# Optimization experiments

Measured on AMD Instinct MI355X. Metric: run time of the kernel, lower is better.

The kernel has to match this reference:

```python
import jax, jax.numpy as jnp
import numpy as np

B, L, C, D = 4, 128, 1024, 512

def setup_inputs() -> dict:
    key = jax.random.key(0)
    ks = jax.random.split(key, 6)
    scale = 1.0 / np.sqrt(D)
    return {
        "hidden": jax.random.normal(ks[0], (B, L, D), dtype=jnp.float32),
        "ctx": jax.random.normal(ks[1], (B, C, D), dtype=jnp.float32),
        "W": jax.random.normal(ks[2], (D, D), dtype=jnp.float32) * scale,
        "U": jax.random.normal(ks[3], (D, D), dtype=jnp.float32) * scale,
        "U_b": jax.random.normal(ks[4], (D,), dtype=jnp.float32) * scale,
        "V": jax.random.normal(ks[5], (D,), dtype=jnp.float32) * scale,
    }

def reference(hidden, ctx, W, U, U_b, V):
    # Bahdanau additive attention: softmax_j V . tanh(W h_i + U c_j + b)
    wq = jnp.einsum('bld,ed->ble', hidden, W)          # [B, L, D]
    uc = jnp.einsum('bcd,ed->bce', ctx, U) + U_b       # [B, C, D]
    s = jnp.tanh(wq[:, :, None, :] + uc[:, None, :, :])  # [B, L, C, D]
    align = jnp.einsum('blcd,d->blc', s, V)            # [B, L, C]
    return jax.nn.softmax(align, axis=-1)
```

## Files before the change

kernel.cpp:

```cpp
#include <hip/hip_runtime.h>
#include <hip/hip_bf16.h>


#define SCALE2 2.8853900817779268f
#define PART (4 * 128 * 1024)

typedef _Float16 f16x8 __attribute__((ext_vector_type(8)));
typedef float f32x4 __attribute__((ext_vector_type(4)));

__device__ __forceinline__ void gload16(const void* g, void* l) {
    __builtin_amdgcn_global_load_lds(
        (const __attribute__((address_space(1))) void*)g,
        (__attribute__((address_space(3))) void*)l,
        16, 0, 0);
}

__global__ __launch_bounds__(256) void gemm_mfma(
    const float* __restrict__ hidden, const float* __restrict__ ctx,
    const float* __restrict__ Wmat, const float* __restrict__ Umat,
    const float* __restrict__ U_b,
    float* __restrict__ ewq_t, float* __restrict__ euc_t)
{
    __shared__ __align__(16) _Float16 Xh[2][64][40];
    __shared__ __align__(16) _Float16 Xl[2][64][40];
    __shared__ __align__(16) _Float16 Wh[2][64][40];
    __shared__ __align__(16) _Float16 Wl[2][64][40];

    const int tid  = threadIdx.x;
    const int lane = tid & 63;
    const int w    = tid >> 6;

    const float *X, *Wm, *bias;
    float* Ct;
    int m0, crow0, Mb, bshift;
    {
        int gb = blockIdx.x;
        if (gb < 64) {
            m0 = (gb & 7) * 64; crow0 = (gb >> 3) * 64;
            X = hidden; Wm = Wmat; bias = nullptr; Ct = ewq_t; Mb = 128; bshift = 7;
        } else {
            int g = gb - 64;
            m0 = (g & 7) * 64; crow0 = (g >> 3) * 64;
            X = ctx; Wm = Umat; bias = U_b; Ct = euc_t; Mb = 1024; bshift = 10;
        }
    }

    const int sr = tid >> 2;
    const int sk = (tid & 3) * 8;
    const float* xsrc = X  + (size_t)(crow0 + sr) * 512 + sk;
    const float* wsrc = Wm + (size_t)(m0    + sr) * 512 + sk;

    f32x4 acc[4];
#pragma unroll
    for (int t = 0; t < 4; ++t) acc[t] = (f32x4){0.f, 0.f, 0.f, 0.f};

    float xrA[8], wrA[8], xrB[8], wrB[8];

#define LOADRAW(xr_, wr_, chunk)                                              \
    {                                                                         \
        float4 a_ = *(const float4*)(xsrc + (chunk) * 32);                    \
        float4 b_ = *(const float4*)(xsrc + (chunk) * 32 + 4);                \
        float4 c_ = *(const float4*)(wsrc + (chunk) * 32);                    \
        float4 d_ = *(const float4*)(wsrc + (chunk) * 32 + 4);                \
        xr_[0]=a_.x; xr_[1]=a_.y; xr_[2]=a_.z; xr_[3]=a_.w;                   \
        xr_[4]=b_.x; xr_[5]=b_.y; xr_[6]=b_.z; xr_[7]=b_.w;                   \
        wr_[0]=c_.x; wr_[1]=c_.y; wr_[2]=c_.z; wr_[3]=c_.w;                   \
        wr_[4]=d_.x; wr_[5]=d_.y; wr_[6]=d_.z; wr_[7]=d_.w;                   \
    }

#define CVTWRITE(xr_, wr_, buf)                                               \
    {                                                                         \
        f16x8 xh_, xl_, wh_, wl_;                                             \
        _Pragma("unroll")                                                     \
        for (int i_ = 0; i_ < 8; ++i_) {                                      \
            xh_[i_] = (_Float16)xr_[i_];                                      \
            xl_[i_] = (_Float16)(xr_[i_] - (float)xh_[i_]);                   \
            wh_[i_] = (_Float16)wr_[i_];                                      \
            wl_[i_] = (_Float16)(wr_[i_] - (float)wh_[i_]);                   \
        }                                                                     \
        *(f16x8*)&Xh[buf][sr][sk] = xh_; *(f16x8*)&Xl[buf][sr][sk] = xl_;     \
        *(f16x8*)&Wh[buf][sr][sk] = wh_; *(f16x8*)&Wl[buf][sr][sk] = wl_;     \
    }

    const int fr = lane & 15;
    const int fk = (lane >> 4) * 8;
    const int mrow = w * 16 + fr;

#define MFMA_CHUNK(bu)                                                        \
    {                                                                         \
        const f16x8 ah = *(const f16x8*)&Wh[bu][mrow][fk];                    \
        const f16x8 al = *(const f16x8*)&Wl[bu][mrow][fk];                    \
        _Pragma("unroll")                                                     \
        for (int t = 0; t < 4; ++t) {                                         \
            const f16x8 bh = *(const f16x8*)&Xh[bu][t * 16 + fr][fk];         \
            const f16x8 bl = *(const f16x8*)&Xl[bu][t * 16 + fr][fk];         \
            acc[t] = __builtin_amdgcn_mfma_f32_16x16x32_f16(ah, bh, acc[t], 0, 0, 0); \
            acc[t] = __builtin_amdgcn_mfma_f32_16x16x32_f16(ah, bl, acc[t], 0, 0, 0); \
            acc[t] = __builtin_amdgcn_mfma_f32_16x16x32_f16(al, bh, acc[t], 0, 0, 0); \
        }                                                                     \
    }

    LOADRAW(xrA, wrA, 0);
    CVTWRITE(xrA, wrA, 0);
    LOADRAW(xrA, wrA, 1);
    __syncthreads();

#define ITER(kc, xP, wP, xQ, wQ)                                              \
    {                                                                         \
        if ((kc) + 2 < 16) LOADRAW(xQ, wQ, (kc) + 2);                         \
        MFMA_CHUNK((kc) & 1);                                                 \
        if ((kc) + 1 < 16) CVTWRITE(xP, wP, ((kc) + 1) & 1);                  \
        __syncthreads();                                                      \
    }

#pragma unroll
    for (int kc2 = 0; kc2 < 16; kc2 += 2) {
        ITER(kc2,     xrA, wrA, xrB, wrB);
        ITER(kc2 + 1, xrB, wrB, xrA, wrA);
    }
#undef ITER
#undef MFMA_CHUNK
#undef CVTWRITE
#undef LOADRAW

    const int rbase = m0 + w * 16 + (lane >> 4) * 4;
    float bl4[4] = {0.f, 0.f, 0.f, 0.f};
    if (bias) {
        float4 t = *(const float4*)&bias[rbase];
        bl4[0] = t.x; bl4[1] = t.y; bl4[2] = t.z; bl4[3] = t.w;
    }
    const int bidx = crow0 >> bshift;
    const int cl0  = crow0 & (Mb - 1);
    float* obase = Ct + ((size_t)bidx * 512 + rbase) * Mb + cl0 + fr;
#pragma unroll
    for (int r = 0; r < 4; ++r)
#pragma unroll
        for (int t = 0; t < 4; ++t)
            obase[(size_t)r * Mb + t * 16] =
                __builtin_amdgcn_exp2f(SCALE2 * (acc[t][r] + bl4[r]));
}

__global__ __launch_bounds__(256) void fused_align11(
    const float* __restrict__ ewq_t,
    const float* __restrict__ euc_t,
    const float* __restrict__ Vv,
    float* __restrict__ pout, float* __restrict__ pws)
{
    __shared__ __align__(16) float uc_s[2][16][256];
    __shared__ __align__(16) float wq_s[2][16][16];
    __shared__ float v_s[64];

    const int tid  = threadIdx.x;
    const int lane = tid & 63;
    const int w    = __builtin_amdgcn_readfirstlane(tid >> 6);
    const int c0   = blockIdx.x * 256;
    const int l0   = blockIdx.y * 16;
    const int z    = blockIdx.z;
    const int b    = z >> 3, h = z & 7;
    const int d0   = h * 64;

    const float* ucb = euc_t + ((size_t)b * 512 + d0) * 1024 + c0;
    const float* wqb = ewq_t + ((size_t)b * 512 + d0) * 128 + l0;

    if (tid < 64) v_s[tid] = Vv[d0 + tid];

#define STAGE(buf, chunk)                                                     \
    {                                                                         \
        _Pragma("unroll")                                                     \
        for (int i_ = 0; i_ < 4; ++i_) {                                      \
            const int d_ = w * 4 + i_;                                        \
            gload16(ucb + (size_t)((chunk) * 16 + d_) * 1024 + lane * 4,      \
                    &uc_s[buf][d_][0]);                                       \
        }                                                                     \
        if (w == 0)                                                           \
            gload16(wqb + (size_t)((chunk) * 16 + (lane >> 2)) * 128 +        \
                        (lane & 3) * 4,                                       \
                    &wq_s[buf][0][0]);                                        \
    }

    float acc[4][4];
#pragma unroll
    for (int i = 0; i < 4; ++i)
#pragma unroll
        for (int k = 0; k < 4; ++k) acc[i][k] = 0.0f;

#define COMPUTE(bu, ch)                                                       \
    do {                                                                      \
        __builtin_amdgcn_s_setprio(1);                                        \
        float vr[16];                                                         \
        _Pragma("unroll")                                                     \
        for (int j_ = 0; j_ < 4; ++j_) {                                      \
            const float4 v4_ = *(const float4*)&v_s[(ch) * 16 + j_ * 4];      \
            vr[j_ * 4 + 0] = v4_.x; vr[j_ * 4 + 1] = v4_.y;                   \
            vr[j_ * 4 + 2] = v4_.z; vr[j_ * 4 + 3] = v4_.w;                   \
        }                                                                     \
        float nn[4][4], dn[4][4];                                             \
        {                                                                     \
            const float4 e = *(const float4*)&uc_s[bu][0][lane * 4];          \
            const float4 q = *(const float4*)&wq_s[bu][0][w * 4];             \
            const float ea[4] = {e.x, e.y, e.z, e.w};                         \
            const float qa[4] = {q.x, q.y, q.z, q.w};                         \
            _Pragma("unroll")                                                 \
            for (int i = 0; i < 4; ++i)                                       \
                _Pragma("unroll")                                             \
                for (int k = 0; k < 4; ++k) {                                 \
                    dn[i][k] = fmaf(qa[i], ea[k], 1.0f);                      \
                    nn[i][k] = vr[0];                                         \
                }                                                             \
        }                                                                     \
        _Pragma("unroll")                                                     \
        for (int dd = 1; dd < 16; ++dd) {                                     \
            const float4 e = *(const float4*)&uc_s[bu][dd][lane * 4];         \
            const float4 q = *(const float4*)&wq_s[bu][dd][w * 4];            \
            const float ea[4] = {e.x, e.y, e.z, e.w};                         \
            const float qa[4] = {q.x, q.y, q.z, q.w};                         \
            const float vv = vr[dd];                                          \
            _Pragma("unroll")                                                 \
            for (int i = 0; i < 4; ++i)                                       \
                _Pragma("unroll")                                             \
                for (int k = 0; k < 4; ++k) {                                 \
                    const float t_ = fmaf(qa[i], ea[k], 1.0f);                \
                    nn[i][k] = fmaf(nn[i][k], t_, vv * dn[i][k]);             \
                    dn[i][k] *= t_;                                           \
                }                                                             \
        }                                                                     \
        _Pragma("unroll")                                                     \
        for (int i = 0; i < 4; ++i)                                           \
            _Pragma("unroll")                                                 \
            for (int k = 0; k < 4; ++k)                                       \
                acc[i][k] = fmaf(nn[i][k],                                    \
                                 __builtin_amdgcn_rcpf(dn[i][k]), acc[i][k]); \
        __builtin_amdgcn_s_setprio(0);                                        \
    } while (0)

    STAGE(0, 0);
    __syncthreads();

    for (int cc = 0; cc < 2; ++cc) {
        STAGE(1, 2 * cc + 1);
        COMPUTE(0, 2 * cc);
        __syncthreads();
        if (cc == 0) STAGE(0, 2);
        COMPUTE(1, 2 * cc + 1);
        __syncthreads();
    }
#undef STAGE
#undef COMPUTE

    float* pp = (h == 0) ? pout : pws + (size_t)(h - 1) * PART;
#pragma unroll
    for (int i = 0; i < 4; ++i) {
        float4 r;
        r.x = -2.0f * acc[i][0]; r.y = -2.0f * acc[i][1];
        r.z = -2.0f * acc[i][2]; r.w = -2.0f * acc[i][3];
        *(float4*)(pp + ((size_t)b * 128 + l0 + w * 4 + i) * 1024 + c0 + lane * 4) = r;
    }
}

__global__ __launch_bounds__(256) void softmax5(
    float* __restrict__ data, const float* __restrict__ pws)
{
    __shared__ float red[8];
    const int row  = blockIdx.x;
    const int tid  = threadIdx.x;
    const int w    = tid >> 6;
    const int lane = tid & 63;
    float* p = data + (size_t)row * 1024;

    float4 x = *(const float4*)(p + tid * 4);
#pragma unroll
    for (int t = 0; t < 7; ++t) {
        const float4 a =
            *(const float4*)(pws + (size_t)t * PART + (size_t)row * 1024 + tid * 4);
        x.x += a.x; x.y += a.y; x.z += a.z; x.w += a.w;
    }

    float m = fmaxf(fmaxf(x.x, x.y), fmaxf(x.z, x.w));
#pragma unroll
    for (int mask = 32; mask >= 1; mask >>= 1) m = fmaxf(m, __shfl_xor(m, mask, 64));
    if (lane == 0) red[w] = m;
    __syncthreads();
    m = fmaxf(fmaxf(red[0], red[1]), fmaxf(red[2], red[3]));

    const float LOG2E = 1.4426950408889634f;
    x.x = __builtin_amdgcn_exp2f((x.x - m) * LOG2E);
    x.y = __builtin_amdgcn_exp2f((x.y - m) * LOG2E);
    x.z = __builtin_amdgcn_exp2f((x.z - m) * LOG2E);
    x.w = __builtin_amdgcn_exp2f((x.w - m) * LOG2E);
    float s = (x.x + x.y) + (x.z + x.w);
#pragma unroll
    for (int mask = 32; mask >= 1; mask >>= 1) s += __shfl_xor(s, mask, 64);
    if (lane == 0) red[4 + w] = s;
    __syncthreads();
    s = (red[4] + red[5]) + (red[6] + red[7]);

    const float r = __builtin_amdgcn_rcpf(s);
    x.x *= r; x.y *= r; x.z *= r; x.w *= r;
    *(float4*)(p + tid * 4) = x;
}

extern "C" void kernel_launch(void* const* d_in, const int* in_sizes, int n_in,
                              void* d_out, int out_size, void* d_ws, size_t ws_size,
                              hipStream_t stream)
{
    const float* hidden = (const float*)d_in[0];
    const float* ctx    = (const float*)d_in[1];
    const float* W      = (const float*)d_in[2];
    const float* U      = (const float*)d_in[3];
    const float* U_b    = (const float*)d_in[4];
    const float* V      = (const float*)d_in[5];
    float* out = (float*)d_out;

    float* ewq_t = (float*)d_ws;
    float* euc_t = ewq_t + 4 * 512 * 128;
    float* pws   = euc_t + 4 * 512 * 1024;

    gemm_mfma<<<576, 256, 0, stream>>>(hidden, ctx, W, U, U_b, ewq_t, euc_t);
    fused_align11<<<dim3(4, 8, 32), 256, 0, stream>>>(ewq_t, euc_t, V, out, pws);
    softmax5<<<512, 256, 0, stream>>>(out, pws);
}
```

Before: 52.87 us.

## Halve per-thread L tile and process d in 8-row chunks with 16 rows per rational group

The fused alignment kernel now gives each thread 2 query rows × 4 context columns instead of 4×4, doubling the grid in the L dimension to 1024 blocks. The d dimension is staged in smaller 8-row chunks with a deeper pipelined loop. The rational (product-of-tanh) accumulation now spans two chunks, 16 d values, before the reciprocal. This lowers register pressure and LDS footprint to raise occupancy and parallelism, and drops the setprio hints. The cost is half the reuse of each loaded uc value and more sync points per block.

Result: slower. 115.2 us (+117.9%).

```diff
diff --git a/kernel.cpp b/kernel.cpp
--- a/kernel.cpp
+++ b/kernel.cpp
@@ -13,6 +13,12 @@
         (const __attribute__((address_space(1))) void*)g,
         (__attribute__((address_space(3))) void*)l,
         16, 0, 0);
+}
+__device__ __forceinline__ void gload4(const void* g, void* l) {
+    __builtin_amdgcn_global_load_lds(
+        (const __attribute__((address_space(1))) void*)g,
+        (__attribute__((address_space(3))) void*)l,
+        4, 0, 0);
 }
 
 __global__ __launch_bounds__(256) void gemm_mfma(
@@ -140,21 +146,21 @@
                 __builtin_amdgcn_exp2f(SCALE2 * (acc[t][r] + bl4[r]));
 }
 
-__global__ __launch_bounds__(256) void fused_align11(
+__global__ __launch_bounds__(256) void fused_align12(
     const float* __restrict__ ewq_t,
     const float* __restrict__ euc_t,
     const float* __restrict__ Vv,
     float* __restrict__ pout, float* __restrict__ pws)
 {
-    __shared__ __align__(16) float uc_s[2][16][256];
-    __shared__ __align__(16) float wq_s[2][16][16];
-    __shared__ float v_s[64];
+    __shared__ __align__(16) float uc_s[2][8][256];
+    __shared__ __align__(16) float wq_s[2][8][8];
+    __shared__ __align__(16) float v_s[64];
 
     const int tid  = threadIdx.x;
     const int lane = tid & 63;
     const int w    = __builtin_amdgcn_readfirstlane(tid >> 6);
     const int c0   = blockIdx.x * 256;
-    const int l0   = blockIdx.y * 16;
+    const int l0   = blockIdx.y * 8;
     const int z    = blockIdx.z;
     const int b    = z >> 3, h = z & 7;
     const int d0   = h * 64;
@@ -164,84 +170,81 @@
 
     if (tid < 64) v_s[tid] = Vv[d0 + tid];
 
-#define STAGE(buf, chunk)                                                     \
+#define STAGE(buf, ch)                                                        \
     {                                                                         \
         _Pragma("unroll")                                                     \
-        for (int i_ = 0; i_ < 4; ++i_) {                                      \
-            const int d_ = w * 4 + i_;                                        \
-            gload16(ucb + (size_t)((chunk) * 16 + d_) * 1024 + lane * 4,      \
-                    &uc_s[buf][d_][0]);                                       \
+        for (int i_ = 0; i_ < 2; ++i_) {                                      \
+            const int r_ = w * 2 + i_;                                        \
+            gload16(ucb + (size_t)((ch) * 8 + r_) * 1024 + lane * 4,          \
+                    &uc_s[buf][r_][0]);                                       \
         }                                                                     \
         if (w == 0)                                                           \
-            gload16(wqb + (size_t)((chunk) * 16 + (lane >> 2)) * 128 +        \
-                        (lane & 3) * 4,                                       \
-                    &wq_s[buf][0][0]);                                        \
-    }
-
-    float acc[4][4];
-#pragma unroll
-    for (int i = 0; i < 4; ++i)
+            gload4(wqb + (size_t)((ch) * 8 + (lane >> 3)) * 128 + (lane & 7), \
+                   &wq_s[buf][0][0]);                                         \
+    }
+
+    float acc[2][4], nn[2][4], dn[2][4];
+#pragma unroll
+    for (int i = 0; i < 2; ++i)
 #pragma unroll
         for (int k = 0; k < 4; ++k) acc[i][k] = 0.0f;
 
-#define COMPUTE(bu, ch)                                                       \
+#define COMPUTE(bu, ch, FIRST, LAST)                                          \
     do {                                                                      \
-        __builtin_amdgcn_s_setprio(1);                                        \
-        float vr[16];                                                         \
+        float vr[8];                                                          \
+        {                                                                     \
+            const float4 v0_ = *(const float4*)&v_s[(ch) * 8];                \
+            const float4 v1_ = *(const float4*)&v_s[(ch) * 8 + 4];            \
+            vr[0]=v0_.x; vr[1]=v0_.y; vr[2]=v0_.z; vr[3]=v0_.w;               \
+            vr[4]=v1_.x; vr[5]=v1_.y; vr[6]=v1_.z; vr[7]=v1_.w;               \
+        }                                                                     \
         _Pragma("unroll")                                                     \
-        for (int j_ = 0; j_ < 4; ++j_) {                                      \
-            const float4 v4_ = *(const float4*)&v_s[(ch) * 16 + j_ * 4];      \
-            vr[j_ * 4 + 0] = v4_.x; vr[j_ * 4 + 1] = v4_.y;                   \
-            vr[j_ * 4 + 2] = v4_.z; vr[j_ * 4 + 3] = v4_.w;                   \
-        }                                                                     \
-        float nn[4][4], dn[4][4];                                             \
-        {                                                                     \
-            const float4 e = *(const float4*)&uc_s[bu][0][lane * 4];          \
-            const float4 q = *(const float4*)&wq_s[bu][0][w * 4];             \
+        for (int dd = 0; dd < 8; ++dd) {                                      \
+            const float4 e = *(const float4*)&uc_s[bu][dd][lane * 4];         \
+            const float2 q = *(const float2*)&wq_s[bu][dd][w * 2];            \
             const float ea[4] = {e.x, e.y, e.z, e.w};                         \
-            const float qa[4] = {q.x, q.y, q.z, q.w};                         \
+            const float qa[2] = {q.x, q.y};                                   \
+            const float vv = vr[dd];                                          \
+            if (FIRST && dd == 0) {                                           \
+                _Pragma("unroll")                                             \
+                for (int i = 0; i < 2; ++i)                                   \
+                    _Pragma("unroll")                                         \
+                    for (int k = 0; k < 4; ++k) {                             \
+                        dn[i][k] = fmaf(qa[i], ea[k], 1.0f);                  \
+                        nn[i][k] = vv;                                        \
+                    }                                                         \
+            } else {                                                          \
+                _Pragma("unroll")                                             \
+                for (int i = 0; i < 2; ++i)                                   \
+                    _Pragma("unroll")                                         \
+                    for (int k = 0; k < 4; ++k) {                             \
+                        const float t_ = fmaf(qa[i], ea[k], 1.0f);            \
+                        nn[i][k] = fmaf(nn[i][k], t_, vv * dn[i][k]);         \
+                        dn[i][k] *= t_;                                       \
+                    }                                                         \
+            }                                                                 \
+        }                                                                     \
+        if (LAST) {                                                           \
             _Pragma("unroll")                                                 \
-            for (int i = 0; i < 4; ++i)                                       \
+            for (int i = 0; i < 2; ++i)                                       \
                 _Pragma("unroll")                                             \
-                for (int k = 0; k < 4; ++k) {                                 \
-                    dn[i][k] = fmaf(qa[i], ea[k], 1.0f);                      \
-                    nn[i][k] = vr[0];                                         \
-                }                                                             \
-        }                                                                     \
-        _Pragma("unroll")                                                     \
-        for (int dd = 1; dd < 16; ++dd) {                                     \
-            const float4 e = *(const float4*)&uc_s[bu][dd][lane * 4];         \
-            const float4 q = *(const float4*)&wq_s[bu][dd][w * 4];            \
-            const float ea[4] = {e.x, e.y, e.z, e.w};                         \
-            const float qa[4] = {q.x, q.y, q.z, q.w};                         \
-            const float vv = vr[dd];                                          \
-            _Pragma("unroll")                                                 \
-            for (int i = 0; i < 4; ++i)                                       \
-                _Pragma("unroll")                                             \
-                for (int k = 0; k < 4; ++k) {                                 \
-                    const float t_ = fmaf(qa[i], ea[k], 1.0f);                \
-                    nn[i][k] = fmaf(nn[i][k], t_, vv * dn[i][k]);             \
-                    dn[i][k] *= t_;                                           \
-                }                                                             \
-        }                                                                     \
-        _Pragma("unroll")                                                     \
-        for (int i = 0; i < 4; ++i)                                           \
-            _Pragma("unroll")                                                 \
-            for (int k = 0; k < 4; ++k)                                       \
-                acc[i][k] = fmaf(nn[i][k],                                    \
-                                 __builtin_amdgcn_rcpf(dn[i][k]), acc[i][k]); \
-        __builtin_amdgcn_s_setprio(0);                                        \
+                for (int k = 0; k < 4; ++k)                                   \
+                    acc[i][k] = fmaf(nn[i][k],                                \
+                                     __builtin_amdgcn_rcpf(dn[i][k]),         \
+                                     acc[i][k]);                              \
+        }                                                                     \
     } while (0)
 
     STAGE(0, 0);
     __syncthreads();
 
-    for (int cc = 0; cc < 2; ++cc) {
+#pragma unroll
+    for (int cc = 0; cc < 4; ++cc) {
         STAGE(1, 2 * cc + 1);
-        COMPUTE(0, 2 * cc);
+        COMPUTE(0, 2 * cc, 1, 0);
         __syncthreads();
-        if (cc == 0) STAGE(0, 2);
-        COMPUTE(1, 2 * cc + 1);
+        if (cc < 3) STAGE(0, 2 * cc + 2);
+        COMPUTE(1, 2 * cc + 1, 0, 1);
         __syncthreads();
     }
 #undef STAGE
@@ -249,11 +252,11 @@
 
     float* pp = (h == 0) ? pout : pws + (size_t)(h - 1) * PART;
 #pragma unroll
-    for (int i = 0; i < 4; ++i) {
+    for (int i = 0; i < 2; ++i) {
         float4 r;
         r.x = -2.0f * acc[i][0]; r.y = -2.0f * acc[i][1];
         r.z = -2.0f * acc[i][2]; r.w = -2.0f * acc[i][3];
-        *(float4*)(pp + ((size_t)b * 128 + l0 + w * 4 + i) * 1024 + c0 + lane * 4) = r;
+        *(float4*)(pp + ((size_t)b * 128 + l0 + w * 2 + i) * 1024 + c0 + lane * 4) = r;
     }
 }
 
@@ -316,6 +319,6 @@
     float* pws   = euc_t + 4 * 512 * 1024;
 
     gemm_mfma<<<576, 256, 0, stream>>>(hidden, ctx, W, U, U_b, ewq_t, euc_t);
-    fused_align11<<<dim3(4, 8, 32), 256, 0, stream>>>(ewq_t, euc_t, V, out, pws);
+    fused_align12<<<dim3(4, 16, 32), 256, 0, stream>>>(ewq_t, euc_t, V, out, pws);
     softmax5<<<512, 256, 0, stream>>>(out, pws);
 }
```

## Combine tanh fractions in groups of four with per-group reciprocal, single-buffer LDS

Applied to the files above, without the earlier changes.

Restructures the additive-attention inner loop. Each group of four d terms is merged into one rational term (N/(A*B)) with its own reciprocal, replacing one running numerator/denominator over 16 d. Staging changes from double-buffered 16-row chunks to two single-buffered 32-row chunks, and the priority hints are dropped. This bounds the product magnitudes and shortens the dependency chains, but adds four times as many reciprocals and removes load/compute overlap.

Result: slower. 84.87 us (+60.5%).

```diff
diff --git a/kernel.cpp b/kernel.cpp
--- a/kernel.cpp
+++ b/kernel.cpp
@@ -140,15 +140,15 @@
                 __builtin_amdgcn_exp2f(SCALE2 * (acc[t][r] + bl4[r]));
 }
 
-__global__ __launch_bounds__(256) void fused_align11(
+__global__ __launch_bounds__(256) void fused_align15(
     const float* __restrict__ ewq_t,
     const float* __restrict__ euc_t,
     const float* __restrict__ Vv,
     float* __restrict__ pout, float* __restrict__ pws)
 {
-    __shared__ __align__(16) float uc_s[2][16][256];
-    __shared__ __align__(16) float wq_s[2][16][16];
-    __shared__ float v_s[64];
+    __shared__ __align__(16) float uc_s[32][256];
+    __shared__ __align__(16) float wq_s[32][16];
+    __shared__ __align__(16) float v_s[64];
 
     const int tid  = threadIdx.x;
     const int lane = tid & 63;
@@ -164,96 +164,85 @@
 
     if (tid < 64) v_s[tid] = Vv[d0 + tid];
 
-#define STAGE(buf, chunk)                                                     \
+#define STAGE(ch)                                                             \
     {                                                                         \
         _Pragma("unroll")                                                     \
-        for (int i_ = 0; i_ < 4; ++i_) {                                      \
-            const int d_ = w * 4 + i_;                                        \
-            gload16(ucb + (size_t)((chunk) * 16 + d_) * 1024 + lane * 4,      \
-                    &uc_s[buf][d_][0]);                                       \
+        for (int i_ = 0; i_ < 8; ++i_) {                                      \
+            const int d_ = w * 8 + i_;                                        \
+            gload16(ucb + (size_t)((ch) * 32 + d_) * 1024 + lane * 4,         \
+                    &uc_s[d_][0]);                                            \
         }                                                                     \
-        if (w == 0)                                                           \
-            gload16(wqb + (size_t)((chunk) * 16 + (lane >> 2)) * 128 +        \
+        if (w < 2)                                                            \
+            gload16(wqb + (size_t)((ch) * 32 + w * 16 + (lane >> 2)) * 128 +  \
                         (lane & 3) * 4,                                       \
-                    &wq_s[buf][0][0]);                                        \
+                    &wq_s[w * 16][0]);                                        \
     }
 
     float acc[4][4];
 #pragma unroll
-    for (int i = 0; i < 4; ++i)
-#pragma unroll
-        for (int k = 0; k < 4; ++k) acc[i][k] = 0.0f;
-
-#define COMPUTE(bu, ch)                                                       \
-    do {                                                                      \
-        __builtin_amdgcn_s_setprio(1);                                        \
-        float vr[16];                                                         \
+    for (int l = 0; l < 4; ++l)
+#pragma unroll
+        for (int k = 0; k < 4; ++k) acc[l][k] = 0.0f;
+
+#define COMPUTE(ch)                                                           \
+    {                                                                         \
         _Pragma("unroll")                                                     \
-        for (int j_ = 0; j_ < 4; ++j_) {                                      \
-            const float4 v4_ = *(const float4*)&v_s[(ch) * 16 + j_ * 4];      \
-            vr[j_ * 4 + 0] = v4_.x; vr[j_ * 4 + 1] = v4_.y;                   \
-            vr[j_ * 4 + 2] = v4_.z; vr[j_ * 4 + 3] = v4_.w;                   \
-        }                                                                     \
-        float nn[4][4], dn[4][4];                                             \
-        {                                                                     \
-            const float4 e = *(const float4*)&uc_s[bu][0][lane * 4];          \
-            const float4 q = *(const float4*)&wq_s[bu][0][w * 4];             \
-            const float ea[4] = {e.x, e.y, e.z, e.w};                         \
-            const float qa[4] = {q.x, q.y, q.z, q.w};                         \
+        for (int qd = 0; qd < 8; ++qd) {                                      \
+            const int dd = qd * 4;                                            \
+            const float4 e0 = *(const float4*)&uc_s[dd + 0][lane * 4];        \
+            const float4 e1 = *(const float4*)&uc_s[dd + 1][lane * 4];        \
+            const float4 e2 = *(const float4*)&uc_s[dd + 2][lane * 4];        \
+            const float4 e3 = *(const float4*)&uc_s[dd + 3][lane * 4];       \
+            const float4 q0 = *(const float4*)&wq_s[dd + 0][w * 4];           \
+            const float4 q1 = *(const float4*)&wq_s[dd + 1][w * 4];           \
+            const float4 q2 = *(const float4*)&wq_s[dd + 2][w * 4];           \
+            const float4 q3 = *(const float4*)&wq_s[dd + 3][w * 4];           \
+            const float4 vq = *(const float4*)&v_s[(ch) * 32 + dd];           \
+            const float e0a[4] = {e0.x, e0.y, e0.z, e0.w};                    \
+            const float e1a[4] = {e1.x, e1.y, e1.z, e1.w};                    \
+            const float e2a[4] = {e2.x, e2.y, e2.z, e2.w};                    \
+            const float e3a[4] = {e3.x, e3.y, e3.z, e3.w};                    \
+            const float q0a[4] = {q0.x, q0.y, q0.z, q0.w};                    \
+            const float q1a[4] = {q1.x, q1.y, q1.z, q1.w};                    \
+            const float q2a[4] = {q2.x, q2.y, q2.z, q2.w};                    \
+            const float q3a[4] = {q3.x, q3.y, q3.z, q3.w};                    \
             _Pragma("unroll")                                                 \
-            for (int i = 0; i < 4; ++i)                                       \
+            for (int l = 0; l < 4; ++l) {                                     \
                 _Pragma("unroll")                                             \
                 for (int k = 0; k < 4; ++k) {                                 \
-                    dn[i][k] = fmaf(qa[i], ea[k], 1.0f);                      \
-                    nn[i][k] = vr[0];                                         \
+                    const float t0 = fmaf(q0a[l], e0a[k], 1.0f);              \
+                    const float t1 = fmaf(q1a[l], e1a[k], 1.0f);              \
+                    const float t2 = fmaf(q2a[l], e2a[k], 1.0f);              \
+                    const float t3 = fmaf(q3a[l], e3a[k], 1.0f);              \
+                    const float A  = t0 * t1;                                 \
+                    const float B  = t2 * t3;                                 \
+                    const float n01 = fmaf(vq.x, t1, vq.y * t0);              \
+                    const float n23 = fmaf(vq.z, t3, vq.w * t2);              \
+                    const float N   = fmaf(n01, B, n23 * A);                  \
+                    acc[l][k] = fmaf(N, __builtin_amdgcn_rcpf(A * B),         \
+                                     acc[l][k]);                              \
                 }                                                             \
+            }                                                                 \
         }                                                                     \
-        _Pragma("unroll")                                                     \
-        for (int dd = 1; dd < 16; ++dd) {                                     \
-            const float4 e = *(const float4*)&uc_s[bu][dd][lane * 4];         \
-            const float4 q = *(const float4*)&wq_s[bu][dd][w * 4];            \
-            const float ea[4] = {e.x, e.y, e.z, e.w};                         \
-            const float qa[4] = {q.x, q.y, q.z, q.w};                         \
-            const float vv = vr[dd];                                          \
-            _Pragma("unroll")                                                 \
-            for (int i = 0; i < 4; ++i)                                       \
-                _Pragma("unroll")                                             \
-                for (int k = 0; k < 4; ++k) {                                 \
-                    const float t_ = fmaf(qa[i], ea[k], 1.0f);                \
-                    nn[i][k] = fmaf(nn[i][k], t_, vv * dn[i][k]);             \
-                    dn[i][k] *= t_;                                           \
-                }                                                             \
-        }                                                                     \
-        _Pragma("unroll")                                                     \
-        for (int i = 0; i < 4; ++i)                                           \
-            _Pragma("unroll")                                                 \
-            for (int k = 0; k < 4; ++k)                                       \
-                acc[i][k] = fmaf(nn[i][k],                                    \
-                                 __builtin_amdgcn_rcpf(dn[i][k]), acc[i][k]); \
-        __builtin_amdgcn_s_setprio(0);                                        \
-    } while (0)
-
-    STAGE(0, 0);
-    __syncthreads();
-
-    for (int cc = 0; cc < 2; ++cc) {
-        STAGE(1, 2 * cc + 1);
-        COMPUTE(0, 2 * cc);
-        __syncthreads();
-        if (cc == 0) STAGE(0, 2);
-        COMPUTE(1, 2 * cc + 1);
-        __syncthreads();
-    }
+    }
+
+    STAGE(0);
+    __syncthreads();
+    COMPUTE(0);
+    __syncthreads();
+    STAGE(1);
+    __syncthreads();
+    COMPUTE(1);
 #undef STAGE
 #undef COMPUTE
 
     float* pp = (h == 0) ? pout : pws + (size_t)(h - 1) * PART;
 #pragma unroll
-    for (int i = 0; i < 4; ++i) {
-        float4 r;
-        r.x = -2.0f * acc[i][0]; r.y = -2.0f * acc[i][1];
-        r.z = -2.0f * acc[i][2]; r.w = -2.0f * acc[i][3];
-        *(float4*)(pp + ((size_t)b * 128 + l0 + w * 4 + i) * 1024 + c0 + lane * 4) = r;
+    for (int l = 0; l < 4; ++l) {
+        float4 o;
+        o.x = -2.0f * acc[l][0]; o.y = -2.0f * acc[l][1];
+        o.z = -2.0f * acc[l][2]; o.w = -2.0f * acc[l][3];
+        *(float4*)(pp + ((size_t)b * 128 + l0 + w * 4 + l) * 1024 + c0 + lane * 4) = o;
     }
 }
 
@@ -294,8 +283,8 @@
     __syncthreads();
     s = (red[4] + red[5]) + (red[6] + red[7]);
 
-    const float r = __builtin_amdgcn_rcpf(s);
-    x.x *= r; x.y *= r; x.z *= r; x.w *= r;
+    const float rr = __builtin_amdgcn_rcpf(s);
+    x.x *= rr; x.y *= rr; x.z *= rr; x.w *= rr;
     *(float4*)(p + tid * 4) = x;
 }
 
@@ -316,6 +305,6 @@
     float* pws   = euc_t + 4 * 512 * 1024;
 
     gemm_mfma<<<576, 256, 0, stream>>>(hidden, ctx, W, U, U_b, ewq_t, euc_t);
-    fused_align11<<<dim3(4, 8, 32), 256, 0, stream>>>(ewq_t, euc_t, V, out, pws);
+    fused_align15<<<dim3(4, 8, 32), 256, 0, stream>>>(ewq_t, euc_t, V, out, pws);
     softmax5<<<512, 256, 0, stream>>>(out, pws);
 }
```
